# Kernel tuning notes

Measured on AMD Instinct MI355X. Metric: run time of the kernel, lower is better.

The kernel has to match this reference:

```python
import jax
jax.config.update("jax_enable_x64", True)
import jax.numpy as jnp
import numpy as np

_N = 100000
_E = 6400000


def _mix(z):
    # splitmix64 finalizer: strong per-element mixing so that summing mixed
    # neighbor colors is a (collision-resistant) commutative multiset hash.
    z = z + jnp.uint64(0x9E3779B97F4A7C15)
    z = (z ^ (z >> jnp.uint64(30))) * jnp.uint64(0xBF58476D1CE4E5B9)
    z = (z ^ (z >> jnp.uint64(27))) * jnp.uint64(0x94D049BB133111EB)
    return z ^ (z >> jnp.uint64(31))


def setup_inputs() -> dict:
    key = jax.random.key(0)
    k1, k2 = jax.random.split(key)
    x = jax.random.randint(k1, (_N,), 0, 50, dtype=jnp.int64)
    edge_index = jax.random.randint(k2, (2, _E), 0, _N, dtype=jnp.int64)
    return {"x": x, "edge_index": edge_index}


def reference(x, edge_index):
    # WL refinement: new_color[i] = ID( (x[i], multiset{x[j] : j in N(i)}) ),
    # IDs assigned in first-seen node order (matches the torch hashmap).
    # The torch code sorts neighbors before hashing, so the result depends
    # only on the neighbor MULTISET; we hash the multiset commutatively via
    # sum of splitmix64-mixed colors (collisions negligible in uint64).
    n = x.shape[0]
    row, col = edge_index[0], edge_index[1]  # neighbors of i: row[e] where col[e]==i
    neigh_hash = jax.ops.segment_sum(_mix(x[row].astype(jnp.uint64)), col,
                                     num_segments=n)  # (n,) uint64
    own = _mix(x.astype(jnp.uint64) ^ jnp.uint64(0xABCD1234DEADBEEF))
    sig = _mix(own + neigh_hash)  # (n,) per-node signature

    # Dedup + relabel in first-occurrence order (deterministic, jit-safe).
    _, inv = jnp.unique(sig, return_inverse=True, size=n, fill_value=jnp.uint64(0))
    inv = inv.reshape(-1)
    first = jax.ops.segment_min(jnp.arange(n, dtype=jnp.int64), inv,
                                num_segments=n)  # first node index per group
    rank = jnp.argsort(jnp.argsort(first))  # group -> first-seen color id
    return rank[inv].astype(jnp.int64)
```

## Files before the change

### kernel.cpp

```cpp
#include <hip/hip_runtime.h>

typedef unsigned long long u64;
typedef unsigned int u32;
typedef unsigned short u16;
typedef unsigned char u8;

#define CAP (1 << 17)
#define CAP_MASK (CAP - 1)
#define EMPTY_KEY 0xFFFFFFFFFFFFFFFFULL

#define TILE 8192
#define NXCD 8
#define NBUCK 196
#define BSHIFT 9
#define BMASK 511
#define CAPB 4608

__device__ __forceinline__ u64 mix64(u64 z) {
    z += 0x9E3779B97F4A7C15ULL;
    z = (z ^ (z >> 30)) * 0xBF58476D1CE4E5B9ULL;
    z = (z ^ (z >> 27)) * 0x94D049BB133111EBULL;
    return z ^ (z >> 31);
}

__global__ void init_ws(u64* __restrict__ neigh, u64* __restrict__ keys,
                        u32* __restrict__ firsts, u32* __restrict__ groupcolor,
                        u32* __restrict__ nodeslot, u32* __restrict__ partials,
                        u32* __restrict__ cursor, u8* __restrict__ xb,
                        const int* __restrict__ x, int n) {
    int i = blockIdx.x * blockDim.x + threadIdx.x;
    keys[i] = EMPTY_KEY;
    firsts[i] = 0xFFFFFFFFu;
    groupcolor[i] = 0u;
    if (i < n) { neigh[i] = 0ULL; nodeslot[i] = 0u; xb[i] = (u8)x[i]; }
    if (i < 512) partials[i] = 0u;
    if (i < NXCD * NBUCK) cursor[i] = 0u;
}

__global__ void scatter_edges(const int* __restrict__ row, const int* __restrict__ col,
                              const u8* __restrict__ xb, u32* __restrict__ cursor,
                              u16* __restrict__ bdata, int E, int n) {
    __shared__ u32 ent[TILE];
    __shared__ u32 lcnt[NBUCK];
    __shared__ u32 lscan[NBUCK];
    __shared__ u32 lbase[NBUCK];
    __shared__ u32 s[512];
    int tid = threadIdx.x;
    int g = blockIdx.x & (NXCD - 1);
    long tile0 = (long)blockIdx.x * TILE;
    if (tid < NBUCK) lcnt[tid] = 0u;
    __syncthreads();

    u32 pk_[16];
    u32 nm = (u32)n - 1u;
    #pragma unroll
    for (int k = 0; k < 4; ++k) {
        long e0 = tile0 + (long)k * 2048 + tid * 4;
        u32 pk0 = 0xFFFFFFFFu, pk1 = 0xFFFFFFFFu, pk2 = 0xFFFFFFFFu, pk3 = 0xFFFFFFFFu;
        if (e0 < (long)E) {
            int4 r4 = *(const int4*)(row + e0);
            int4 c4 = *(const int4*)(col + e0);
            u32 c0 = min((u32)c4.x, nm), c1 = min((u32)c4.y, nm);
            u32 c2 = min((u32)c4.z, nm), c3 = min((u32)c4.w, nm);
            u32 v0 = xb[min((u32)r4.x, nm)] & 63u, v1 = xb[min((u32)r4.y, nm)] & 63u;
            u32 v2 = xb[min((u32)r4.z, nm)] & 63u, v3 = xb[min((u32)r4.w, nm)] & 63u;
            pk0 = ((c0 >> BSHIFT) << 16) | ((c0 & BMASK) << 6) | v0;
            pk1 = ((c1 >> BSHIFT) << 16) | ((c1 & BMASK) << 6) | v1;
            pk2 = ((c2 >> BSHIFT) << 16) | ((c2 & BMASK) << 6) | v2;
            pk3 = ((c3 >> BSHIFT) << 16) | ((c3 & BMASK) << 6) | v3;
            atomicAdd(&lcnt[pk0 >> 16], 1u);
            atomicAdd(&lcnt[pk1 >> 16], 1u);
            atomicAdd(&lcnt[pk2 >> 16], 1u);
            atomicAdd(&lcnt[pk3 >> 16], 1u);
        }
        pk_[k * 4 + 0] = pk0; pk_[k * 4 + 1] = pk1;
        pk_[k * 4 + 2] = pk2; pk_[k * 4 + 3] = pk3;
    }
    __syncthreads();

    u32 v = (tid < NBUCK) ? lcnt[tid] : 0u;
    s[tid] = v;
    __syncthreads();
    for (int d = 1; d < 512; d <<= 1) {
        u32 a = (tid >= d) ? s[tid - d] : 0u;
        __syncthreads();
        s[tid] += a;
        __syncthreads();
    }
    if (tid < NBUCK) {
        lscan[tid] = s[tid] - v;
        if (v) lbase[tid] = atomicAdd(&cursor[g * NBUCK + tid], v);
        lcnt[tid] = 0u;
    }
    __syncthreads();

    #pragma unroll
    for (int k = 0; k < 16; ++k) {
        u32 pk = pk_[k];
        if (pk != 0xFFFFFFFFu) {
            u32 b = pk >> 16;
            u32 pos = lscan[b] + atomicAdd(&lcnt[b], 1u);
            ent[pos] = pk;
        }
    }
    __syncthreads();

    int valid = (int)min((long)TILE, (long)E - tile0);
    for (int j = tid; j < valid; j += 512) {
        u32 pk = ent[j];
        u32 b = pk >> 16;
        u32 dst = lbase[b] + ((u32)j - lscan[b]);
        if (dst < CAPB)
            bdata[((size_t)g * NBUCK + b) * CAPB + dst] = (u16)pk;
    }
}

__global__ void bucket_reduce(const u32* __restrict__ cursor, const u16* __restrict__ bdata,
                              u64* __restrict__ neigh, int n) {
    int b = blockIdx.x;
    __shared__ u64 acc[512];
    __shared__ u64 mtab[64];
    int tid = threadIdx.x;
    if (tid < 64) mtab[tid] = mix64((u64)tid);
    if (tid < 512) acc[tid] = 0ULL;
    __syncthreads();
    for (int g = 0; g < NXCD; ++g) {
        u32 cnt = min(cursor[g * NBUCK + b], (u32)CAPB);
        const u16* seg = bdata + ((size_t)g * NBUCK + b) * CAPB;
        for (u32 i = tid; i < cnt; i += 1024) {
            u32 p = (u32)seg[i];
            atomicAdd(&acc[(p >> 6) & 511u], mtab[p & 63u]);
        }
    }
    __syncthreads();
    if (tid < 512) {
        int node = b * 512 + tid;
        if (node < n) neigh[node] = acc[tid];
    }
}

__global__ void edge_kernel(const int* __restrict__ row, const int* __restrict__ col,
                            const int* __restrict__ x, u64* __restrict__ neigh,
                            int nedges, int n) {
    int t = blockIdx.x * blockDim.x + threadIdx.x;
    int e = t * 4;
    u32 nm = (u32)n - 1u;
    if (e + 3 < nedges) {
        int4 r4 = *(const int4*)(row + e);
        int4 c4 = *(const int4*)(col + e);
        u32 r0 = min((u32)r4.x, nm), c0 = min((u32)c4.x, nm);
        u32 r1 = min((u32)r4.y, nm), c1 = min((u32)c4.y, nm);
        u32 r2 = min((u32)r4.z, nm), c2 = min((u32)c4.z, nm);
        u32 r3 = min((u32)r4.w, nm), c3 = min((u32)c4.w, nm);
        atomicAdd(&neigh[c0], mix64((u64)(u32)x[r0]));
        atomicAdd(&neigh[c1], mix64((u64)(u32)x[r1]));
        atomicAdd(&neigh[c2], mix64((u64)(u32)x[r2]));
        atomicAdd(&neigh[c3], mix64((u64)(u32)x[r3]));
    } else {
        for (int k = e; k < nedges; ++k) {
            u32 r = min((u32)row[k], nm);
            u32 c = min((u32)col[k], nm);
            atomicAdd(&neigh[c], mix64((u64)(u32)x[r]));
        }
    }
}

__global__ void sig_insert(const int* __restrict__ x, const u64* __restrict__ neigh,
                           u64* __restrict__ keys, u32* __restrict__ firsts,
                           u32* __restrict__ nodeslot, int n) {
    int i = blockIdx.x * blockDim.x + threadIdx.x;
    if (i >= n) return;
    u64 own = mix64(((u64)(u32)x[i]) ^ 0xABCD1234DEADBEEFULL);
    u64 sig = mix64(own + neigh[i]);
    u32 h = (u32)(sig ^ (sig >> 32)) & CAP_MASK;
    for (int p = 0; p < CAP; ++p) {
        u64 old = atomicCAS(&keys[h], EMPTY_KEY, sig);
        if (old == EMPTY_KEY || old == sig) break;
        h = (h + 1) & CAP_MASK;
    }
    atomicMin(&firsts[h], (u32)i);
    nodeslot[i] = h;
}

__global__ void flags_blocksum(const u32* __restrict__ firsts, const u32* __restrict__ nodeslot,
                               u32* __restrict__ partials, int n) {
    __shared__ u32 sdata[256];
    int tid = threadIdx.x;
    int i = blockIdx.x * 256 + tid;
    u32 f = 0;
    if (i < n) f = (firsts[nodeslot[i] & CAP_MASK] == (u32)i) ? 1u : 0u;
    sdata[tid] = f;
    __syncthreads();
    for (int sft = 128; sft > 0; sft >>= 1) {
        if (tid < sft) sdata[tid] += sdata[tid + sft];
        __syncthreads();
    }
    if (tid == 0) partials[blockIdx.x] = sdata[0];
}

__global__ void scan_partials(u32* __restrict__ partials, int nb) {
    __shared__ u32 s[512];
    int t = threadIdx.x;
    u32 v = (t < nb) ? partials[t] : 0;
    s[t] = v;
    __syncthreads();
    for (int d = 1; d < 512; d <<= 1) {
        u32 a = (t >= d) ? s[t - d] : 0;
        __syncthreads();
        s[t] += a;
        __syncthreads();
    }
    if (t < nb) partials[t] = s[t] - v;
}

__global__ void assign_colors(const u32* __restrict__ firsts, const u32* __restrict__ nodeslot,
                              const u32* __restrict__ partials, u32* __restrict__ groupcolor, int n) {
    __shared__ u32 sdata[256];
    int tid = threadIdx.x;
    int i = blockIdx.x * 256 + tid;
    u32 f = 0, slot = 0;
    if (i < n) {
        slot = nodeslot[i] & CAP_MASK;
        f = (firsts[slot] == (u32)i) ? 1u : 0u;
    }
    sdata[tid] = f;
    __syncthreads();
    for (int d = 1; d < 256; d <<= 1) {
        u32 a = (tid >= d) ? sdata[tid - d] : 0;
        __syncthreads();
        sdata[tid] += a;
        __syncthreads();
    }
    u32 exc = sdata[tid] - f + partials[blockIdx.x];
    if (i < n && f) groupcolor[slot] = exc;
}

__global__ void write_out(const u32* __restrict__ nodeslot, const u32* __restrict__ groupcolor,
                          int* __restrict__ out, int n) {
    int i = blockIdx.x * blockDim.x + threadIdx.x;
    if (i < n) {
        u32 g = groupcolor[nodeslot[i] & CAP_MASK];
        g = min(g, (u32)(n - 1));
        out[i] = (int)g;
    }
}

extern "C" void kernel_launch(void* const* d_in, const int* in_sizes, int n_in,
                              void* d_out, int out_size, void* d_ws, size_t ws_size,
                              hipStream_t stream) {
    const int* x = (const int*)d_in[0];
    const int* ei = (const int*)d_in[1];
    int n = in_sizes[0];
    int E = in_sizes[1] / 2;
    const int* row = ei;
    const int* col = ei + E;

    char* base = (char*)d_ws;
    size_t off = 0;
    auto take = [&](size_t bytes) -> char* {
        char* p = base + off;
        off += (bytes + 255) & ~(size_t)255;
        return p;
    };
    u64* neigh      = (u64*)take((size_t)n * 8);
    u64* keys       = (u64*)take((size_t)CAP * 8);
    u32* firsts     = (u32*)take((size_t)CAP * 4);
    u32* groupcolor = (u32*)take((size_t)CAP * 4);
    u32* nodeslot   = (u32*)take((size_t)n * 4);
    u32* partials   = (u32*)take((size_t)512 * 4);
    u8*  xb         = (u8*)take((size_t)n);
    u32* cursor     = (u32*)take((size_t)NXCD * NBUCK * 4);
    u16* bdata      = (u16*)take((size_t)NXCD * NBUCK * CAPB * 2);
    bool binned = (off <= ws_size);

    int nb = (n + 255) / 256;

    init_ws<<<CAP / 256, 256, 0, stream>>>(neigh, keys, firsts, groupcolor, nodeslot,
                                           partials, cursor, xb, x, n);
    if (binned) {
        int tiles = (E + TILE - 1) / TILE;
        scatter_edges<<<tiles, 512, 0, stream>>>(row, col, xb, cursor, bdata, E, n);
        bucket_reduce<<<NBUCK, 1024, 0, stream>>>(cursor, bdata, neigh, n);
    } else {
        edge_kernel<<<(E / 4 + 255) / 256, 256, 0, stream>>>(row, col, x, neigh, E, n);
    }
    sig_insert<<<(n + 255) / 256, 256, 0, stream>>>(x, neigh, keys, firsts, nodeslot, n);
    flags_blocksum<<<nb, 256, 0, stream>>>(firsts, nodeslot, partials, n);
    scan_partials<<<1, 512, 0, stream>>>(partials, nb);
    assign_colors<<<nb, 256, 0, stream>>>(firsts, nodeslot, partials, groupcolor, n);
    write_out<<<(n + 255) / 256, 256, 0, stream>>>(nodeslot, groupcolor, (int*)d_out, n);
}
```

Baseline: 199.2 us.

## Double hash table capacity, alias groupcolor onto keys, insert two nodes per thread

The signature hash table grows to 2^18 slots, which lowers the load factor and shortens linear-probe chains. The separate groupcolor buffer and its initialization are removed; groupcolor now reuses the keys storage, which is no longer needed by the time colors are assigned. sig_insert handles two nodes per thread and interleaves their atomicCAS probes so more atomic latency is in flight per thread. The cost is a larger table to initialize and scan, plus half as many threads doing the inserts.

```diff
diff --git a/kernel.cpp b/kernel.cpp
--- a/kernel.cpp
+++ b/kernel.cpp
@@ -5,7 +5,7 @@
 typedef unsigned short u16;
 typedef unsigned char u8;
 
-#define CAP (1 << 17)
+#define CAP (1 << 18)
 #define CAP_MASK (CAP - 1)
 #define EMPTY_KEY 0xFFFFFFFFFFFFFFFFULL
 
@@ -24,14 +24,12 @@
 }
 
 __global__ void init_ws(u64* __restrict__ neigh, u64* __restrict__ keys,
-                        u32* __restrict__ firsts, u32* __restrict__ groupcolor,
-                        u32* __restrict__ nodeslot, u32* __restrict__ partials,
-                        u32* __restrict__ cursor, u8* __restrict__ xb,
-                        const int* __restrict__ x, int n) {
+                        u32* __restrict__ firsts, u32* __restrict__ nodeslot,
+                        u32* __restrict__ partials, u32* __restrict__ cursor,
+                        u8* __restrict__ xb, const int* __restrict__ x, int n) {
     int i = blockIdx.x * blockDim.x + threadIdx.x;
     keys[i] = EMPTY_KEY;
     firsts[i] = 0xFFFFFFFFu;
-    groupcolor[i] = 0u;
     if (i < n) { neigh[i] = 0ULL; nodeslot[i] = 0u; xb[i] = (u8)x[i]; }
     if (i < 512) partials[i] = 0u;
     if (i < NXCD * NBUCK) cursor[i] = 0u;
@@ -167,19 +165,35 @@
 
 __global__ void sig_insert(const int* __restrict__ x, const u64* __restrict__ neigh,
                            u64* __restrict__ keys, u32* __restrict__ firsts,
-                           u32* __restrict__ nodeslot, int n) {
+                           u32* __restrict__ nodeslot, int n, int half) {
     int i = blockIdx.x * blockDim.x + threadIdx.x;
-    if (i >= n) return;
-    u64 own = mix64(((u64)(u32)x[i]) ^ 0xABCD1234DEADBEEFULL);
-    u64 sig = mix64(own + neigh[i]);
-    u32 h = (u32)(sig ^ (sig >> 32)) & CAP_MASK;
-    for (int p = 0; p < CAP; ++p) {
-        u64 old = atomicCAS(&keys[h], EMPTY_KEY, sig);
-        if (old == EMPTY_KEY || old == sig) break;
-        h = (h + 1) & CAP_MASK;
-    }
-    atomicMin(&firsts[h], (u32)i);
-    nodeslot[i] = h;
+    int j = i + half;
+    bool va = (i < half);
+    bool vb = (j < n);
+    u64 sa = 0, sb = 0;
+    u32 ha = 0, hb = 0;
+    if (va) {
+        u64 own = mix64(((u64)(u32)x[i]) ^ 0xABCD1234DEADBEEFULL);
+        sa = mix64(own + neigh[i]);
+        ha = (u32)(sa ^ (sa >> 32)) & CAP_MASK;
+    }
+    if (vb) {
+        u64 own = mix64(((u64)(u32)x[j]) ^ 0xABCD1234DEADBEEFULL);
+        sb = mix64(own + neigh[j]);
+        hb = (u32)(sb ^ (sb >> 32)) & CAP_MASK;
+    }
+    bool da = !va, db = !vb;
+    for (int p = 0; p < CAP && !(da && db); ++p) {
+        u64 oa, ob;
+        if (!da) oa = atomicCAS(&keys[ha], EMPTY_KEY, sa);
+        if (!db) ob = atomicCAS(&keys[hb], EMPTY_KEY, sb);
+        if (!da) { if (oa == EMPTY_KEY || oa == sa) da = true; else ha = (ha + 1) & CAP_MASK; }
+        if (!db) { if (ob == EMPTY_KEY || ob == sb) db = true; else hb = (hb + 1) & CAP_MASK; }
+    }
+    if (va) atomicMin(&firsts[ha], (u32)i);
+    if (vb) atomicMin(&firsts[hb], (u32)j);
+    if (va) nodeslot[i] = ha;
+    if (vb) nodeslot[j] = hb;
 }
 
 __global__ void flags_blocksum(const u32* __restrict__ firsts, const u32* __restrict__ nodeslot,
@@ -265,17 +279,18 @@
     u64* neigh      = (u64*)take((size_t)n * 8);
     u64* keys       = (u64*)take((size_t)CAP * 8);
     u32* firsts     = (u32*)take((size_t)CAP * 4);
-    u32* groupcolor = (u32*)take((size_t)CAP * 4);
     u32* nodeslot   = (u32*)take((size_t)n * 4);
     u32* partials   = (u32*)take((size_t)512 * 4);
     u8*  xb         = (u8*)take((size_t)n);
     u32* cursor     = (u32*)take((size_t)NXCD * NBUCK * 4);
     u16* bdata      = (u16*)take((size_t)NXCD * NBUCK * CAPB * 2);
+    u32* groupcolor = (u32*)keys;
     bool binned = (off <= ws_size);
 
     int nb = (n + 255) / 256;
-
-    init_ws<<<CAP / 256, 256, 0, stream>>>(neigh, keys, firsts, groupcolor, nodeslot,
+    int half = (n + 1) / 2;
+
+    init_ws<<<CAP / 256, 256, 0, stream>>>(neigh, keys, firsts, nodeslot,
                                            partials, cursor, xb, x, n);
     if (binned) {
         int tiles = (E + TILE - 1) / TILE;
@@ -284,7 +299,7 @@
     } else {
         edge_kernel<<<(E / 4 + 255) / 256, 256, 0, stream>>>(row, col, x, neigh, E, n);
     }
-    sig_insert<<<(n + 255) / 256, 256, 0, stream>>>(x, neigh, keys, firsts, nodeslot, n);
+    sig_insert<<<(half + 255) / 256, 256, 0, stream>>>(x, neigh, keys, firsts, nodeslot, n, half);
     flags_blocksum<<<nb, 256, 0, stream>>>(firsts, nodeslot, partials, n);
     scan_partials<<<1, 512, 0, stream>>>(partials, nb);
     assign_colors<<<nb, 256, 0, stream>>>(firsts, nodeslot, partials, groupcolor, n);
```

Result: faster. 161.6 us (-18.8%).
